# Performance work log

Hardware: AMD Instinct MI355X
Metric: run time of the kernel (lower is better)

## Reference

```python
import jax, jax.numpy as jnp
import numpy as np

B, L, D = 4, 2048, 512
H = 8
DK = 512 // H  # 64
DV = 512 // H  # 64
TEMP = float(np.power(DK, 0.5))
LN_EPS = 1e-5


def setup_inputs() -> dict:
    key = jax.random.key(0)
    ks = jax.random.split(key, 12)
    s = 0.02
    return {
        "q": jax.random.normal(ks[0], (B, L, D), jnp.float32),
        "k": jax.random.normal(ks[1], (B, L, D), jnp.float32),
        "v": jax.random.normal(ks[2], (B, L, D), jnp.float32),
        "mask": jax.random.randint(ks[3], (B, L, L), 0, 2, jnp.int32),
        "wq_w": jax.random.normal(ks[4], (H * DK, D), jnp.float32) * s,
        "wq_b": jnp.zeros((H * DK,), jnp.float32),
        "wv_w": jax.random.normal(ks[5], (H * DV, D), jnp.float32) * s,
        "wv_b": jnp.zeros((H * DV,), jnp.float32),
        "fc_w": jax.random.normal(ks[6], (D, H * DV), jnp.float32) * s,
        "fc_b": jnp.zeros((D,), jnp.float32),
        "ln_g": jnp.ones((D,), jnp.float32),
        "ln_b": jnp.zeros((D,), jnp.float32),
    }


def reference(q, k, v, mask, wq_w, wq_b, wv_w, wv_b, fc_w, fc_b, ln_g, ln_b):
    residual = q
    # NOTE: source module projects k with w_qs (bug preserved faithfully)
    qh = (q @ wq_w.T + wq_b).reshape(B, L, H, DK).transpose(0, 2, 1, 3)  # bhld
    kh = (k @ wq_w.T + wq_b).reshape(B, L, H, DK).transpose(0, 2, 1, 3)
    vh = (v @ wv_w.T + wv_b).reshape(B, L, H, DV).transpose(0, 2, 1, 3)
    attn = jnp.einsum("bhqd,bhkd->bhqk", qh / TEMP, kh)
    attn = jnp.where(mask[:, None, :, :] == 1, -1e9, attn)
    attn = jax.nn.softmax(attn, axis=-1)
    out = jnp.einsum("bhqk,bhkd->bhqd", attn, vh)  # (B, H, L, DV)
    # faithful buffer reinterpretation: .view(n_head, sz_b, L, DV)
    out = out.reshape(H, B, L, DV).transpose(0, 2, 1, 3).reshape(B, L, H * DV)
    out = out @ fc_w.T + fc_b
    x = out + residual
    mu = jnp.mean(x, axis=-1, keepdims=True)
    var = jnp.mean(jnp.square(x - mu), axis=-1, keepdims=True)
    y = (x - mu) / jnp.sqrt(var + LN_EPS) * ln_g + ln_b
    return (y, attn)
```

## Files before the change

kernel.cpp:

```cpp
#include <hip/hip_runtime.h>

#define NB 4
#define NL 2048
#define ND 512
#define NH 8
#define NTOK (NB * NL)

constexpr float LN_EPS = 1e-5f;

typedef __attribute__((ext_vector_type(8))) short bf16x8;
typedef __attribute__((ext_vector_type(4))) float f32x4;

static __device__ __forceinline__ unsigned short f2bf(float f) {
  unsigned u = __builtin_bit_cast(unsigned, f);
  unsigned r = (u + 0x7fffu + ((u >> 16) & 1u)) >> 16;
  return (unsigned short)r;
}

static __device__ __forceinline__ uint2 pk4(const float4 f) {
  uint2 r;
  r.x = (unsigned)f2bf(f.x) | ((unsigned)f2bf(f.y) << 16);
  r.y = (unsigned)f2bf(f.z) | ((unsigned)f2bf(f.w) << 16);
  return r;
}

__global__ __launch_bounds__(256) void cvt3_bf16(const float* __restrict__ s0,
                                                 const float* __restrict__ s1,
                                                 const float* __restrict__ s2,
                                                 unsigned short* __restrict__ d0,
                                                 unsigned short* __restrict__ d1,
                                                 unsigned short* __restrict__ d2) {
  const float* s = (blockIdx.y == 0) ? s0 : (blockIdx.y == 1) ? s1 : s2;
  unsigned short* d = (blockIdx.y == 0) ? d0 : (blockIdx.y == 1) ? d1 : d2;
  const size_t i = ((size_t)blockIdx.x * 256 + threadIdx.x) * 8;
  const float4 a = *(const float4*)&s[i];
  const float4 b = *(const float4*)&s[i + 4];
  uint4 o;
  const uint2 lo = pk4(a), hi = pk4(b);
  o.x = lo.x; o.y = lo.y; o.z = hi.x; o.w = hi.y;
  *(uint4*)&d[i] = o;
}

__global__ __launch_bounds__(256) void pack_mask(const int* __restrict__ mask,
                                                 unsigned long long* __restrict__ mpk) {
  const int w = threadIdx.x >> 6, lane = threadIdx.x & 63;
  const size_t g = (size_t)blockIdx.x * 4 + w;
  const int m = mask[g * 64 + lane];
  const unsigned long long bits = __ballot(m == 1);
  if (lane == 0) mpk[g] = bits;
}

#define GEMM128_PRELUDE                                                        \
  __shared__ unsigned short As[2][128 * 72];                                   \
  __shared__ unsigned short Bs[2][64 * 72];                                    \
  const int tid = threadIdx.x;                                                 \
  const int w = tid >> 6;                                                      \
  const int lane = tid & 63;                                                   \
  const int quad = lane >> 4, l15 = lane & 15;                                 \
  const int m0 = blockIdx.x * 128, n0 = blockIdx.y * 64;                       \
  const int arow = tid >> 1;                                       \
  const int acol = (tid & 1) * 32;                     \
  const int brow = tid >> 2;                                        \
  const int bcol = (tid & 3) * 16;                                             \
  f32x4 acc[2][4];                                                             \
  _Pragma("unroll") for (int mr = 0; mr < 2; ++mr)                             \
  _Pragma("unroll") for (int nt = 0; nt < 4; ++nt)                             \
    acc[mr][nt] = (f32x4){0.f, 0.f, 0.f, 0.f};                                 \
  uint4 ar[4], br[2];

#define GEMM128_STORE_LDS(buf)                                                 \
  do {                                                                         \
    _Pragma("unroll") for (int j = 0; j < 4; ++j)                              \
      *(uint4*)&As[buf][arow * 72 + acol + j * 8] = ar[j];                     \
    *(uint4*)&Bs[buf][brow * 72 + bcol] = br[0];                               \
    *(uint4*)&Bs[buf][brow * 72 + bcol + 8] = br[1];                           \
  } while (0)

#define GEMM128_COMPUTE(buf)                                                   \
  do {                                                                         \
    _Pragma("unroll") for (int ks = 0; ks < 2; ++ks) {                         \
      const bf16x8 af0 = *(const bf16x8*)&As[buf][(w * 32 + l15) * 72 + ks * 32 + quad * 8]; \
      const bf16x8 af1 = *(const bf16x8*)&As[buf][(w * 32 + 16 + l15) * 72 + ks * 32 + quad * 8]; \
      _Pragma("unroll") for (int nt = 0; nt < 4; ++nt) {                       \
        const bf16x8 bfr = *(const bf16x8*)&Bs[buf][(nt * 16 + l15) * 72 + ks * 32 + quad * 8]; \
        acc[0][nt] = __builtin_amdgcn_mfma_f32_16x16x32_bf16(af0, bfr, acc[0][nt], 0, 0, 0); \
        acc[1][nt] = __builtin_amdgcn_mfma_f32_16x16x32_bf16(af1, bfr, acc[1][nt], 0, 0, 0); \
      }                                                                        \
    }                                                                          \
  } while (0)

#define GEMM128_LOADB(k0)                                                      \
  do {                                                                         \
    br[0] = *(const uint4*)&W[(size_t)(n0 + brow) * ND + (k0) + bcol];         \
    br[1] = *(const uint4*)&W[(size_t)(n0 + brow) * ND + (k0) + bcol + 8];     \
  } while (0)

__global__ __launch_bounds__(256) void gemm_qk_mfma(const unsigned short* __restrict__ X,
                                                    const unsigned short* __restrict__ W,
                                                    const float* __restrict__ bias,
                                                    unsigned short* __restrict__ out,
                                                    float scale) {
  GEMM128_PRELUDE
#define LOADA_QK(k0)                                                           \
  do {                                                                         \
    _Pragma("unroll") for (int j = 0; j < 4; ++j)                              \
      ar[j] = *(const uint4*)&X[(size_t)(m0 + arow) * ND + (k0) + acol + j * 8]; \
  } while (0)
  LOADA_QK(0);
  GEMM128_LOADB(0);
#pragma unroll
  for (int t = 0; t < 8; ++t) {
    const int buf = t & 1;
    GEMM128_STORE_LDS(buf);
    __syncthreads();
    if (t < 7) {
      LOADA_QK((t + 1) * 64);
      GEMM128_LOADB((t + 1) * 64);
    }
    GEMM128_COMPUTE(buf);
  }
#undef LOADA_QK
  const int hh = n0 >> 6;
#pragma unroll
  for (int mr = 0; mr < 2; ++mr)
#pragma unroll
    for (int nt = 0; nt < 4; ++nt) {
      const float b = bias[n0 + nt * 16 + l15];
#pragma unroll
      for (int r = 0; r < 4; ++r)
        As[0][(w * 32 + mr * 16 + quad * 4 + r) * 72 + nt * 16 + l15] =
            f2bf((acc[mr][nt][r] + b) * scale);
    }
  __syncthreads();
  const int tok = m0 + arow;
  const int bb = tok >> 11, l = tok & 2047;
  unsigned short* orow = out + (((size_t)bb * NH + hh) * NL + l) * 64;
#pragma unroll
  for (int j = 0; j < 4; ++j)
    *(uint4*)&orow[acol + j * 8] = *(const uint4*)&As[0][arow * 72 + acol + j * 8];
}

__global__ __launch_bounds__(256) void gemm_v_mfma_t(const unsigned short* __restrict__ X,
                                                     const unsigned short* __restrict__ W,
                                                     const float* __restrict__ bias,
                                                     unsigned short* __restrict__ outT) {
  GEMM128_PRELUDE
#define LOADA_V(k0)                                                            \
  do {                                                                         \
    _Pragma("unroll") for (int j = 0; j < 4; ++j)                              \
      ar[j] = *(const uint4*)&X[(size_t)(m0 + arow) * ND + (k0) + acol + j * 8]; \
  } while (0)
  LOADA_V(0);
  GEMM128_LOADB(0);
#pragma unroll
  for (int t = 0; t < 8; ++t) {
    const int buf = t & 1;
    GEMM128_STORE_LDS(buf);
    __syncthreads();
    if (t < 7) {
      LOADA_V((t + 1) * 64);
      GEMM128_LOADB((t + 1) * 64);
    }
    GEMM128_COMPUTE(buf);
  }
#undef LOADA_V
  const int hh = n0 >> 6;
  unsigned short* T = &As[0][0];
#pragma unroll
  for (int mr = 0; mr < 2; ++mr)
#pragma unroll
    for (int nt = 0; nt < 4; ++nt) {
      const float b = bias[n0 + nt * 16 + l15];
#pragma unroll
      for (int r = 0; r < 4; ++r)
        T[(nt * 16 + l15) * 136 + (w * 32 + mr * 16 + quad * 4 + r)] =
            f2bf(acc[mr][nt][r] + b);
    }
  __syncthreads();
  const int bb = m0 >> 11, l0 = m0 & 2047;
  const int d = tid >> 2;
  const int lcol = (tid & 3) * 32;
  unsigned short* orow = outT + (((size_t)bb * NH + hh) * 64 + d) * NL + l0;
#pragma unroll
  for (int j = 0; j < 4; ++j)
    *(uint4*)&orow[lcol + j * 8] = *(const uint4*)&T[d * 136 + lcol + j * 8];
}

__global__ __launch_bounds__(256) void attn_mfma(const unsigned short* __restrict__ qh,
                                                 const unsigned short* __restrict__ kh,
                                                 const unsigned short* __restrict__ vT,
                                                 const unsigned long long* __restrict__ mpk,
                                                 float* __restrict__ attn,
                                                 unsigned short* __restrict__ ao) {
  const int b = blockIdx.z, h = blockIdx.y, q0 = blockIdx.x * 64;
  const int bh = b * NH + h;
  __shared__ unsigned short Ks[64 * 72];
  __shared__ unsigned short Vt[64 * 72];
  __shared__ unsigned short Ps[4 * 16 * 72];
  const int tid = threadIdx.x;
  const int w = tid >> 6, lane = tid & 63;
  const int quad = lane >> 4, l15 = lane & 15;

  const size_t qoff = ((size_t)bh * NL + q0 + w * 16 + l15) * 64 + quad * 8;
  const bf16x8 aq0 = *(const bf16x8*)(qh + qoff);
  const bf16x8 aq1 = *(const bf16x8*)(qh + qoff + 32);

  const int srow = tid >> 2;
  const int scol = (tid & 3) * 16;

  const size_t kbase = ((size_t)bh * NL + srow) * 64 + scol;
  const size_t vbase = ((size_t)bh * 64 + srow) * NL + scol;
  const size_t mrowq = ((size_t)b * NL + q0 + w * 16 + quad * 4) * 32;

  float rinv[4] = {0.f, 0.f, 0.f, 0.f};

  {
    uint4 kr0 = *(const uint4*)(kh + kbase);
    uint4 kr1 = *(const uint4*)(kh + kbase + 8);
    unsigned long long mqr[4];
#pragma unroll
    for (int r = 0; r < 4; ++r) mqr[r] = mpk[mrowq + (size_t)r * 32];

    for (int kt = 0; kt < 32; ++kt) {
      __syncthreads();
      *(uint4*)&Ks[srow * 72 + scol] = kr0;
      *(uint4*)&Ks[srow * 72 + scol + 8] = kr1;
      __syncthreads();
      unsigned int mb = 0;
#pragma unroll
      for (int r = 0; r < 4; ++r) {
        const unsigned long long t = mqr[r] >> l15;
        mb |= ((unsigned)t & 1u) << (0 + r);
        mb |= (((unsigned)t >> 16) & 1u) << (4 + r);
        mb |= (((unsigned)(t >> 32)) & 1u) << (8 + r);
        mb |= (((unsigned)(t >> 48)) & 1u) << (12 + r);
      }
      if (kt < 31) {
        const size_t kb2 = kbase + (size_t)(kt + 1) * 64 * 64;
        kr0 = *(const uint4*)(kh + kb2);
        kr1 = *(const uint4*)(kh + kb2 + 8);
#pragma unroll
        for (int r = 0; r < 4; ++r) mqr[r] = mpk[mrowq + (size_t)r * 32 + kt + 1];
      }
      f32x4 s[4];
#pragma unroll
      for (int nt = 0; nt < 4; ++nt) {
        const bf16x8 b0 = *(const bf16x8*)&Ks[(nt * 16 + l15) * 72 + quad * 8];
        const bf16x8 b1 = *(const bf16x8*)&Ks[(nt * 16 + l15) * 72 + 32 + quad * 8];
        f32x4 a2 = {0.f, 0.f, 0.f, 0.f};
        a2 = __builtin_amdgcn_mfma_f32_16x16x32_bf16(aq0, b0, a2, 0, 0, 0);
        a2 = __builtin_amdgcn_mfma_f32_16x16x32_bf16(aq1, b1, a2, 0, 0, 0);
        s[nt] = a2;
      }
#pragma unroll
      for (int r = 0; r < 4; ++r)
#pragma unroll
        for (int nt = 0; nt < 4; ++nt) {
          const float e = ((mb >> (nt * 4 + r)) & 1u) ? 0.f : exp2f(s[nt][r]);
          rinv[r] += e;
        }
    }
  }
#pragma unroll
  for (int r = 0; r < 4; ++r) {
    float v = rinv[r];
    v += __shfl_xor(v, 1);
    v += __shfl_xor(v, 2);
    v += __shfl_xor(v, 4);
    v += __shfl_xor(v, 8);
    rinv[r] = 1.0f / v;
  }

  f32x4 oacc[4];
#pragma unroll
  for (int nt = 0; nt < 4; ++nt) oacc[nt] = (f32x4){0.f, 0.f, 0.f, 0.f};

  {
    uint4 kr0 = *(const uint4*)(kh + kbase);
    uint4 kr1 = *(const uint4*)(kh + kbase + 8);
    uint4 vr0 = *(const uint4*)(vT + vbase);
    uint4 vr1 = *(const uint4*)(vT + vbase + 8);
    unsigned long long mqr[4];
#pragma unroll
    for (int r = 0; r < 4; ++r) mqr[r] = mpk[mrowq + (size_t)r * 32];

    for (int kt = 0; kt < 32; ++kt) {
      __syncthreads();
      *(uint4*)&Ks[srow * 72 + scol] = kr0;
      *(uint4*)&Ks[srow * 72 + scol + 8] = kr1;
      *(uint4*)&Vt[srow * 72 + scol] = vr0;
      *(uint4*)&Vt[srow * 72 + scol + 8] = vr1;
      __syncthreads();
      unsigned int mb = 0;
#pragma unroll
      for (int r = 0; r < 4; ++r) {
        const unsigned long long t = mqr[r] >> l15;
        mb |= ((unsigned)t & 1u) << (0 + r);
        mb |= (((unsigned)t >> 16) & 1u) << (4 + r);
        mb |= (((unsigned)(t >> 32)) & 1u) << (8 + r);
        mb |= (((unsigned)(t >> 48)) & 1u) << (12 + r);
      }
      if (kt < 31) {
        const size_t kb2 = kbase + (size_t)(kt + 1) * 64 * 64;
        const size_t vb2 = vbase + (size_t)(kt + 1) * 64;
        kr0 = *(const uint4*)(kh + kb2);
        kr1 = *(const uint4*)(kh + kb2 + 8);
        vr0 = *(const uint4*)(vT + vb2);
        vr1 = *(const uint4*)(vT + vb2 + 8);
#pragma unroll
        for (int r = 0; r < 4; ++r) mqr[r] = mpk[mrowq + (size_t)r * 32 + kt + 1];
      }
      f32x4 s[4];
#pragma unroll
      for (int nt = 0; nt < 4; ++nt) {
        const bf16x8 b0 = *(const bf16x8*)&Ks[(nt * 16 + l15) * 72 + quad * 8];
        const bf16x8 b1 = *(const bf16x8*)&Ks[(nt * 16 + l15) * 72 + 32 + quad * 8];
        f32x4 a2 = {0.f, 0.f, 0.f, 0.f};
        a2 = __builtin_amdgcn_mfma_f32_16x16x32_bf16(aq0, b0, a2, 0, 0, 0);
        a2 = __builtin_amdgcn_mfma_f32_16x16x32_bf16(aq1, b1, a2, 0, 0, 0);
        s[nt] = a2;
      }
#pragma unroll
      for (int r = 0; r < 4; ++r) {
        const int q = q0 + w * 16 + quad * 4 + r;
        float* arow = attn + ((size_t)bh * NL + q) * NL + kt * 64;
        unsigned short* prow = &Ps[(w * 16 + quad * 4 + r) * 72];
#pragma unroll
        for (int nt = 0; nt < 4; ++nt) {
          float e = ((mb >> (nt * 4 + r)) & 1u) ? 0.f : exp2f(s[nt][r]) * rinv[r];
          arow[nt * 16 + l15] = e;
          prow[nt * 16 + l15] = f2bf(e);
        }
      }
      const bf16x8 pa0 = *(const bf16x8*)&Ps[(w * 16 + l15) * 72 + quad * 8];
      const bf16x8 pa1 = *(const bf16x8*)&Ps[(w * 16 + l15) * 72 + 32 + quad * 8];
#pragma unroll
      for (int nt = 0; nt < 4; ++nt) {
        const bf16x8 vb0 = *(const bf16x8*)&Vt[(nt * 16 + l15) * 72 + quad * 8];
        const bf16x8 vb1 = *(const bf16x8*)&Vt[(nt * 16 + l15) * 72 + 32 + quad * 8];
        oacc[nt] = __builtin_amdgcn_mfma_f32_16x16x32_bf16(pa0, vb0, oacc[nt], 0, 0, 0);
        oacc[nt] = __builtin_amdgcn_mfma_f32_16x16x32_bf16(pa1, vb1, oacc[nt], 0, 0, 0);
      }
    }
  }
#pragma unroll
  for (int nt = 0; nt < 4; ++nt)
#pragma unroll
    for (int r = 0; r < 4; ++r)
      Ps[(w * 16 + quad * 4 + r) * 72 + nt * 16 + l15] = f2bf(oacc[nt][r]);
  const int erow = lane >> 2;
  const int ecol = (lane & 3) * 16;
  unsigned short* orow = ao + (((size_t)bh * NL + q0 + w * 16 + erow) * 64) + ecol;
  *(uint4*)&orow[0] = *(const uint4*)&Ps[(w * 16 + erow) * 72 + ecol];
  *(uint4*)&orow[8] = *(const uint4*)&Ps[(w * 16 + erow) * 72 + ecol + 8];
}

__global__ __launch_bounds__(256) void fc_gather_mfma(const unsigned short* __restrict__ AO,
                                                      const unsigned short* __restrict__ W,
                                                      const float* __restrict__ bias,
                                                      const float* __restrict__ resid,
                                                      float* __restrict__ Xout) {
  GEMM128_PRELUDE
  const int nrow = m0 + arow;
  const int b_out = nrow >> 11;
  const int l_out = nrow & 2047;
  const int h2 = b_out * 2 + (l_out >> 10);
  const int q2base = (l_out & 1023) << 1;
#define LOADA_FC(k0)                                                           \
  do {                                                                         \
    const int q2 = q2base | (((k0) >> 8) & 1);                                 \
    const int b2 = ((k0) >> 6) & 3;                                            \
    const unsigned short* abase = AO + ((size_t)(h2 * 4 + b2) * NL + q2) * 64; \
    _Pragma("unroll") for (int j = 0; j < 4; ++j)                              \
      ar[j] = *(const uint4*)&abase[acol + j * 8];                             \
  } while (0)
  LOADA_FC(0);
  GEMM128_LOADB(0);
#pragma unroll
  for (int t = 0; t < 8; ++t) {
    const int buf = t & 1;
    GEMM128_STORE_LDS(buf);
    __syncthreads();
    if (t < 7) {
      LOADA_FC((t + 1) * 64);
      GEMM128_LOADB((t + 1) * 64);
    }
    GEMM128_COMPUTE(buf);
  }
#undef LOADA_FC
#pragma unroll
  for (int mr = 0; mr < 2; ++mr)
#pragma unroll
    for (int nt = 0; nt < 4; ++nt) {
      const float b = bias[n0 + nt * 16 + l15];
#pragma unroll
      for (int r = 0; r < 4; ++r) {
        const int row = m0 + w * 32 + mr * 16 + quad * 4 + r;
        const int col = n0 + nt * 16 + l15;
        const float rv = resid[(size_t)row * ND + col];
        Xout[(size_t)row * ND + col] = acc[mr][nt][r] + b + rv;
      }
    }
}

__global__ __launch_bounds__(256) void layernorm_k(const float* __restrict__ x,
                                                   const float* __restrict__ g,
                                                   const float* __restrict__ bta,
                                                   float* __restrict__ y) {
  const int n = blockIdx.x * 4 + (threadIdx.x >> 6);
  const int lane = threadIdx.x & 63;
  const float* row = x + (size_t)n * ND;
  const float4 a = *(const float4*)&row[lane * 8];
  const float4 c = *(const float4*)&row[lane * 8 + 4];
  float s = a.x + a.y + a.z + a.w + c.x + c.y + c.z + c.w;
  float sq = a.x * a.x + a.y * a.y + a.z * a.z + a.w * a.w +
             c.x * c.x + c.y * c.y + c.z * c.z + c.w * c.w;
#pragma unroll
  for (int off = 32; off; off >>= 1) {
    s += __shfl_down(s, off);
    sq += __shfl_down(sq, off);
  }
  s = __shfl(s, 0);
  sq = __shfl(sq, 0);
  const float mu = s * (1.f / 512.f);
  const float var = sq * (1.f / 512.f) - mu * mu;
  const float rstd = rsqrtf(var + LN_EPS);
  float* yo = y + (size_t)n * ND;
  const int c0 = lane * 8;
  float4 o1, o2;
  o1.x = (a.x - mu) * rstd * g[c0 + 0] + bta[c0 + 0];
  o1.y = (a.y - mu) * rstd * g[c0 + 1] + bta[c0 + 1];
  o1.z = (a.z - mu) * rstd * g[c0 + 2] + bta[c0 + 2];
  o1.w = (a.w - mu) * rstd * g[c0 + 3] + bta[c0 + 3];
  o2.x = (c.x - mu) * rstd * g[c0 + 4] + bta[c0 + 4];
  o2.y = (c.y - mu) * rstd * g[c0 + 5] + bta[c0 + 5];
  o2.z = (c.z - mu) * rstd * g[c0 + 6] + bta[c0 + 6];
  o2.w = (c.w - mu) * rstd * g[c0 + 7] + bta[c0 + 7];
  *(float4*)&yo[c0] = o1;
  *(float4*)&yo[c0 + 4] = o2;
}

extern "C" void kernel_launch(void* const* d_in, const int* in_sizes, int n_in,
                              void* d_out, int out_size, void* d_ws, size_t ws_size,
                              hipStream_t stream) {
  const float* q = (const float*)d_in[0];
  const float* k = (const float*)d_in[1];
  const float* v = (const float*)d_in[2];
  const int* mask = (const int*)d_in[3];
  const float* wq_w = (const float*)d_in[4];
  const float* wq_b = (const float*)d_in[5];
  const float* wv_w = (const float*)d_in[6];
  const float* wv_b = (const float*)d_in[7];
  const float* fc_w = (const float*)d_in[8];
  const float* fc_b = (const float*)d_in[9];
  const float* ln_g = (const float*)d_in[10];
  const float* ln_b = (const float*)d_in[11];

  float* y = (float*)d_out;
  float* attn = y + (size_t)NTOK * ND;

  const size_t SZ = (size_t)NTOK * ND;
  const size_t WSZ = (size_t)ND * ND;
  unsigned short* qhb = (unsigned short*)d_ws;
  unsigned short* khb = qhb + SZ;
  unsigned short* vTb = khb + SZ;
  unsigned short* aob = vTb + SZ;
  unsigned short* qb = aob + SZ;
  unsigned short* kb = qb + SZ;
  unsigned short* vb = kb + SZ;
  float* xx = (float*)(vb + SZ);
  unsigned short* wqb = (unsigned short*)(xx + SZ);
  unsigned short* wvb = wqb + WSZ;
  unsigned short* fcwb = wvb + WSZ;
  unsigned long long* mpk = (unsigned long long*)(fcwb + WSZ);

  cvt3_bf16<<<dim3(SZ / 2048, 3), 256, 0, stream>>>(q, k, v, qb, kb, vb);
  cvt3_bf16<<<dim3(WSZ / 2048, 3), 256, 0, stream>>>(wq_w, wv_w, fc_w, wqb, wvb, fcwb);
  pack_mask<<<(NB * NL * 32) / 4, 256, 0, stream>>>(mask, mpk);

  const dim3 gproj(NTOK / 128, ND / 64);
  gemm_qk_mfma<<<gproj, 256, 0, stream>>>(qb, wqb, wq_b, qhb, 0.125f * 1.44269504f);
  gemm_qk_mfma<<<gproj, 256, 0, stream>>>(kb, wqb, wq_b, khb, 1.0f);
  gemm_v_mfma_t<<<gproj, 256, 0, stream>>>(vb, wvb, wv_b, vTb);
  attn_mfma<<<dim3(NL / 64, NH, NB), 256, 0, stream>>>(qhb, khb, vTb, mpk, attn, aob);
  fc_gather_mfma<<<gproj, 256, 0, stream>>>(aob, fcwb, fc_b, q, xx);
  layernorm_k<<<NTOK / 4, 256, 0, stream>>>(xx, ln_g, ln_b, y);
}
```

Measured before the change: 849.5 us.

## Double attention query tile to 128 rows and single-buffer GEMM LDS

The attention kernel now processes 128 query rows per block with 512 threads, so each K/V tile staged in shared memory is reused by twice as many waves, and each thread loads half as much. The projection GEMMs drop their double-buffered LDS arrays for a single buffer guarded by an extra barrier, halving their shared memory footprint to allow more resident blocks. The intent is to cut K/V global traffic in attention and raise GEMM occupancy. The cost is an added barrier per GEMM iteration and fewer attention blocks in the grid.

After: 899.6 us. 1.06x slower.

```diff
diff --git a/kernel.cpp b/kernel.cpp
--- a/kernel.cpp
+++ b/kernel.cpp
@@ -51,8 +51,8 @@
 }
 
 #define GEMM128_PRELUDE                                                        \
-  __shared__ unsigned short As[2][128 * 72];                                   \
-  __shared__ unsigned short Bs[2][64 * 72];                                    \
+  __shared__ unsigned short As[128 * 72];                                      \
+  __shared__ unsigned short Bs[64 * 72];                                       \
   const int tid = threadIdx.x;                                                 \
   const int w = tid >> 6;                                                      \
   const int lane = tid & 63;                                                   \
@@ -68,21 +68,21 @@
     acc[mr][nt] = (f32x4){0.f, 0.f, 0.f, 0.f};                                 \
   uint4 ar[4], br[2];
 
-#define GEMM128_STORE_LDS(buf)                                                 \
+#define GEMM128_STORE_LDS                                                      \
   do {                                                                         \
     _Pragma("unroll") for (int j = 0; j < 4; ++j)                              \
-      *(uint4*)&As[buf][arow * 72 + acol + j * 8] = ar[j];                     \
-    *(uint4*)&Bs[buf][brow * 72 + bcol] = br[0];                               \
-    *(uint4*)&Bs[buf][brow * 72 + bcol + 8] = br[1];                           \
-  } while (0)
-
-#define GEMM128_COMPUTE(buf)                                                   \
+      *(uint4*)&As[arow * 72 + acol + j * 8] = ar[j];                          \
+    *(uint4*)&Bs[brow * 72 + bcol] = br[0];                                    \
+    *(uint4*)&Bs[brow * 72 + bcol + 8] = br[1];                                \
+  } while (0)
+
+#define GEMM128_COMPUTE                                                        \
   do {                                                                         \
     _Pragma("unroll") for (int ks = 0; ks < 2; ++ks) {                         \
-      const bf16x8 af0 = *(const bf16x8*)&As[buf][(w * 32 + l15) * 72 + ks * 32 + quad * 8]; \
-      const bf16x8 af1 = *(const bf16x8*)&As[buf][(w * 32 + 16 + l15) * 72 + ks * 32 + quad * 8]; \
+      const bf16x8 af0 = *(const bf16x8*)&As[(w * 32 + l15) * 72 + ks * 32 + quad * 8]; \
+      const bf16x8 af1 = *(const bf16x8*)&As[(w * 32 + 16 + l15) * 72 + ks * 32 + quad * 8]; \
       _Pragma("unroll") for (int nt = 0; nt < 4; ++nt) {                       \
-        const bf16x8 bfr = *(const bf16x8*)&Bs[buf][(nt * 16 + l15) * 72 + ks * 32 + quad * 8]; \
+        const bf16x8 bfr = *(const bf16x8*)&Bs[(nt * 16 + l15) * 72 + ks * 32 + quad * 8]; \
         acc[0][nt] = __builtin_amdgcn_mfma_f32_16x16x32_bf16(af0, bfr, acc[0][nt], 0, 0, 0); \
         acc[1][nt] = __builtin_amdgcn_mfma_f32_16x16x32_bf16(af1, bfr, acc[1][nt], 0, 0, 0); \
       }                                                                        \
@@ -94,6 +94,20 @@
     br[0] = *(const uint4*)&W[(size_t)(n0 + brow) * ND + (k0) + bcol];         \
     br[1] = *(const uint4*)&W[(size_t)(n0 + brow) * ND + (k0) + bcol + 8];     \
   } while (0)
+
+#define GEMM128_LOOP(LOADA)                                                    \
+  LOADA(0);                                                                    \
+  GEMM128_LOADB(0);                                                            \
+  _Pragma("unroll") for (int t = 0; t < 8; ++t) {                              \
+    __syncthreads();                     \
+    GEMM128_STORE_LDS;                                                         \
+    __syncthreads();                                                           \
+    if (t < 7) {                                                               \
+      LOADA((t + 1) * 64);                                                     \
+      GEMM128_LOADB((t + 1) * 64);                                             \
+    }                                                                          \
+    GEMM128_COMPUTE;                                                           \
+  }
 
 __global__ __launch_bounds__(256) void gemm_qk_mfma(const unsigned short* __restrict__ X,
                                                     const unsigned short* __restrict__ W,
@@ -106,21 +120,10 @@
     _Pragma("unroll") for (int j = 0; j < 4; ++j)                              \
       ar[j] = *(const uint4*)&X[(size_t)(m0 + arow) * ND + (k0) + acol + j * 8]; \
   } while (0)
-  LOADA_QK(0);
-  GEMM128_LOADB(0);
-#pragma unroll
-  for (int t = 0; t < 8; ++t) {
-    const int buf = t & 1;
-    GEMM128_STORE_LDS(buf);
-    __syncthreads();
-    if (t < 7) {
-      LOADA_QK((t + 1) * 64);
-      GEMM128_LOADB((t + 1) * 64);
-    }
-    GEMM128_COMPUTE(buf);
-  }
+  GEMM128_LOOP(LOADA_QK)
 #undef LOADA_QK
   const int hh = n0 >> 6;
+  __syncthreads();
 #pragma unroll
   for (int mr = 0; mr < 2; ++mr)
 #pragma unroll
@@ -128,7 +131,7 @@
       const float b = bias[n0 + nt * 16 + l15];
 #pragma unroll
       for (int r = 0; r < 4; ++r)
-        As[0][(w * 32 + mr * 16 + quad * 4 + r) * 72 + nt * 16 + l15] =
+        As[(w * 32 + mr * 16 + quad * 4 + r) * 72 + nt * 16 + l15] =
             f2bf((acc[mr][nt][r] + b) * scale);
     }
   __syncthreads();
@@ -137,7 +140,7 @@
   unsigned short* orow = out + (((size_t)bb * NH + hh) * NL + l) * 64;
 #pragma unroll
   for (int j = 0; j < 4; ++j)
-    *(uint4*)&orow[acol + j * 8] = *(const uint4*)&As[0][arow * 72 + acol + j * 8];
+    *(uint4*)&orow[acol + j * 8] = *(const uint4*)&As[arow * 72 + acol + j * 8];
 }
 
 __global__ __launch_bounds__(256) void gemm_v_mfma_t(const unsigned short* __restrict__ X,
@@ -150,22 +153,11 @@
     _Pragma("unroll") for (int j = 0; j < 4; ++j)                              \
       ar[j] = *(const uint4*)&X[(size_t)(m0 + arow) * ND + (k0) + acol + j * 8]; \
   } while (0)
-  LOADA_V(0);
-  GEMM128_LOADB(0);
-#pragma unroll
-  for (int t = 0; t < 8; ++t) {
-    const int buf = t & 1;
-    GEMM128_STORE_LDS(buf);
-    __syncthreads();
-    if (t < 7) {
-      LOADA_V((t + 1) * 64);
-      GEMM128_LOADB((t + 1) * 64);
-    }
-    GEMM128_COMPUTE(buf);
-  }
+  GEMM128_LOOP(LOADA_V)
 #undef LOADA_V
   const int hh = n0 >> 6;
-  unsigned short* T = &As[0][0];
+  unsigned short* T = &As[0];
+  __syncthreads();
 #pragma unroll
   for (int mr = 0; mr < 2; ++mr)
 #pragma unroll
@@ -186,17 +178,17 @@
     *(uint4*)&orow[lcol + j * 8] = *(const uint4*)&T[d * 136 + lcol + j * 8];
 }
 
-__global__ __launch_bounds__(256) void attn_mfma(const unsigned short* __restrict__ qh,
+__global__ __launch_bounds__(512) void attn_mfma(const unsigned short* __restrict__ qh,
                                                  const unsigned short* __restrict__ kh,
                                                  const unsigned short* __restrict__ vT,
                                                  const unsigned long long* __restrict__ mpk,
                                                  float* __restrict__ attn,
                                                  unsigned short* __restrict__ ao) {
-  const int b = blockIdx.z, h = blockIdx.y, q0 = blockIdx.x * 64;
+  const int b = blockIdx.z, h = blockIdx.y, q0 = blockIdx.x * 128;
   const int bh = b * NH + h;
   __shared__ unsigned short Ks[64 * 72];
   __shared__ unsigned short Vt[64 * 72];
-  __shared__ unsigned short Ps[4 * 16 * 72];
+  __shared__ unsigned short Ps[8 * 16 * 72];
   const int tid = threadIdx.x;
   const int w = tid >> 6, lane = tid & 63;
   const int quad = lane >> 4, l15 = lane & 15;
@@ -205,8 +197,8 @@
   const bf16x8 aq0 = *(const bf16x8*)(qh + qoff);
   const bf16x8 aq1 = *(const bf16x8*)(qh + qoff + 32);
 
-  const int srow = tid >> 2;
-  const int scol = (tid & 3) * 16;
+  const int srow = tid >> 3;
+  const int scol = (tid & 7) * 8;
 
   const size_t kbase = ((size_t)bh * NL + srow) * 64 + scol;
   const size_t vbase = ((size_t)bh * 64 + srow) * NL + scol;
@@ -215,16 +207,14 @@
   float rinv[4] = {0.f, 0.f, 0.f, 0.f};
 
   {
-    uint4 kr0 = *(const uint4*)(kh + kbase);
-    uint4 kr1 = *(const uint4*)(kh + kbase + 8);
+    uint4 kr = *(const uint4*)(kh + kbase);
     unsigned long long mqr[4];
 #pragma unroll
     for (int r = 0; r < 4; ++r) mqr[r] = mpk[mrowq + (size_t)r * 32];
 
     for (int kt = 0; kt < 32; ++kt) {
       __syncthreads();
-      *(uint4*)&Ks[srow * 72 + scol] = kr0;
-      *(uint4*)&Ks[srow * 72 + scol + 8] = kr1;
+      *(uint4*)&Ks[srow * 72 + scol] = kr;
       __syncthreads();
       unsigned int mb = 0;
 #pragma unroll
@@ -236,9 +226,7 @@
         mb |= (((unsigned)(t >> 48)) & 1u) << (12 + r);
       }
       if (kt < 31) {
-        const size_t kb2 = kbase + (size_t)(kt + 1) * 64 * 64;
-        kr0 = *(const uint4*)(kh + kb2);
-        kr1 = *(const uint4*)(kh + kb2 + 8);
+        kr = *(const uint4*)(kh + kbase + (size_t)(kt + 1) * 64 * 64);
 #pragma unroll
         for (int r = 0; r < 4; ++r) mqr[r] = mpk[mrowq + (size_t)r * 32 + kt + 1];
       }
@@ -276,20 +264,16 @@
   for (int nt = 0; nt < 4; ++nt) oacc[nt] = (f32x4){0.f, 0.f, 0.f, 0.f};
 
   {
-    uint4 kr0 = *(const uint4*)(kh + kbase);
-    uint4 kr1 = *(const uint4*)(kh + kbase + 8);
-    uint4 vr0 = *(const uint4*)(vT + vbase);
-    uint4 vr1 = *(const uint4*)(vT + vbase + 8);
+    uint4 kr = *(const uint4*)(kh + kbase);
+    uint4 vr = *(const uint4*)(vT + vbase);
     unsigned long long mqr[4];
 #pragma unroll
     for (int r = 0; r < 4; ++r) mqr[r] = mpk[mrowq + (size_t)r * 32];
 
     for (int kt = 0; kt < 32; ++kt) {
       __syncthreads();
-      *(uint4*)&Ks[srow * 72 + scol] = kr0;
-      *(uint4*)&Ks[srow * 72 + scol + 8] = kr1;
-      *(uint4*)&Vt[srow * 72 + scol] = vr0;
-      *(uint4*)&Vt[srow * 72 + scol + 8] = vr1;
+      *(uint4*)&Ks[srow * 72 + scol] = kr;
+      *(uint4*)&Vt[srow * 72 + scol] = vr;
       __syncthreads();
       unsigned int mb = 0;
 #pragma unroll
@@ -301,12 +285,8 @@
         mb |= (((unsigned)(t >> 48)) & 1u) << (12 + r);
       }
       if (kt < 31) {
-        const size_t kb2 = kbase + (size_t)(kt + 1) * 64 * 64;
-        const size_t vb2 = vbase + (size_t)(kt + 1) * 64;
-        kr0 = *(const uint4*)(kh + kb2);
-        kr1 = *(const uint4*)(kh + kb2 + 8);
-        vr0 = *(const uint4*)(vT + vb2);
-        vr1 = *(const uint4*)(vT + vb2 + 8);
+        kr = *(const uint4*)(kh + kbase + (size_t)(kt + 1) * 64 * 64);
+        vr = *(const uint4*)(vT + vbase + (size_t)(kt + 1) * 64);
 #pragma unroll
         for (int r = 0; r < 4; ++r) mqr[r] = mpk[mrowq + (size_t)r * 32 + kt + 1];
       }
@@ -374,19 +354,7 @@
     _Pragma("unroll") for (int j = 0; j < 4; ++j)                              \
       ar[j] = *(const uint4*)&abase[acol + j * 8];                             \
   } while (0)
-  LOADA_FC(0);
-  GEMM128_LOADB(0);
-#pragma unroll
-  for (int t = 0; t < 8; ++t) {
-    const int buf = t & 1;
-    GEMM128_STORE_LDS(buf);
-    __syncthreads();
-    if (t < 7) {
-      LOADA_FC((t + 1) * 64);
-      GEMM128_LOADB((t + 1) * 64);
-    }
-    GEMM128_COMPUTE(buf);
-  }
+  GEMM128_LOOP(LOADA_FC)
 #undef LOADA_FC
 #pragma unroll
   for (int mr = 0; mr < 2; ++mr)
@@ -482,7 +450,7 @@
   gemm_qk_mfma<<<gproj, 256, 0, stream>>>(qb, wqb, wq_b, qhb, 0.125f * 1.44269504f);
   gemm_qk_mfma<<<gproj, 256, 0, stream>>>(kb, wqb, wq_b, khb, 1.0f);
   gemm_v_mfma_t<<<gproj, 256, 0, stream>>>(vb, wvb, wv_b, vTb);
-  attn_mfma<<<dim3(NL / 64, NH, NB), 256, 0, stream>>>(qhb, khb, vTb, mpk, attn, aob);
+  attn_mfma<<<dim3(NL / 128, NH, NB), 512, 0, stream>>>(qhb, khb, vTb, mpk, attn, aob);
   fc_gather_mfma<<<gproj, 256, 0, stream>>>(aob, fcwb, fc_b, q, xx);
   layernorm_k<<<NTOK / 4, 256, 0, stream>>>(xx, ln_g, ln_b, y);
 }
```
